# Kernel optimization log

Measured on AMD Instinct MI355X. Metric: run time of the kernel, lower is better.

## Reference

```python
import jax, jax.numpy as jnp
import numpy as np

# dims: B=batch, S=seq len, H=heads, D=in_features per head, R=realizations, K=conv kernel
B, S, H, D, R, K = 2, 1024, 8, 64, 32, 128


def setup_inputs() -> dict:
    key = jax.random.key(0)
    kq, kk, kwq, kwk, kz = jax.random.split(key, 5)
    queries = jax.random.normal(kq, (B, S, H, D), jnp.float32)
    keys = jax.random.normal(kk, (B, S, H, D), jnp.float32)
    # depthwise conv weights, torch init: uniform[0,1), shape (C_out, 1, K) with groups=C_out
    wq = jax.random.uniform(kwq, (H * D, 1, K), jnp.float32)
    wk = jax.random.uniform(kwk, (H * D, 1, K), jnp.float32)
    # stochastic process noise z: (B*R, H*D, 4K+S), scaled by 1/sqrt(R*D)
    z = jax.random.normal(kz, (B * R, H * D, 4 * K + S), jnp.float32) / np.float32(np.sqrt(R * D))
    return {"queries": queries, "keys": keys, "wq": wq, "wk": wk, "z": z}


def _dwconv(x, w):
    # depthwise 1D cross-correlation, VALID padding (matches nn.Conv1d, groups=C)
    return jax.lax.conv_general_dilated(
        x, w, window_strides=(1,), padding='VALID',
        dimension_numbers=('NCH', 'OIH', 'NCH'),
        feature_group_count=w.shape[0])


def reference(queries, keys, wq, wk, z):
    # note the faithful swap from the source: kbar uses conv_q, qbar uses conv_k
    kbar = _dwconv(z, wq)[:, :, K:K + S].reshape(B, R, H, D, S)
    qbar = _dwconv(z, wk)[:, :, K:K + S].reshape(B, R, H, D, S)
    # fused broadcast-multiply + feature-dim reduction:
    # (qbar * queries[:,None]).sum(axis=3) then permute -> (B,S,H,R)
    qhat = jnp.einsum('brhds,bshd->bshr', qbar, queries)
    khat = jnp.einsum('brhds,bshd->bshr', kbar, keys)
    return qhat, khat
```

## Files before the change

### kernel.cpp

```cpp
#include <hip/hip_runtime.h>

#define BB 2
#define SS 1024
#define HH 8
#define DD 64
#define RR 32
#define KK 128
#define ZLEN 1536
#define HD 512

#define MS 256
#define DC 16
#define NTC 24
#define WROWS 192
#define WSEG (WROWS*DC)
#define PARTS_FLOATS (256*8*2*64*16)

typedef _Float16 f16x8 __attribute__((ext_vector_type(8)));
typedef _Float16 f16x2 __attribute__((ext_vector_type(2)));
typedef float    f32x16 __attribute__((ext_vector_type(16)));

__global__ __launch_bounds__(1024) void convspe_mfma(
    const float* __restrict__ q, const float* __restrict__ kmat,
    const float* __restrict__ wq, const float* __restrict__ wk,
    const float* __restrict__ z, float* __restrict__ parts)
{
    __shared__ __align__(16) _Float16 zbuf[2][16 * 32 * 16];
    __shared__ __align__(16) _Float16 wqs[WSEG];
    __shared__ __align__(16) _Float16 wks[WSEG];

    const int tid  = threadIdx.x;
    const int wv   = tid >> 6;
    const int ssub = __builtin_amdgcn_readfirstlane(wv & 7);
    const int half = __builtin_amdgcn_readfirstlane(wv >> 3);
    const int lane = tid & 63;
    const int rl   = lane & 31;
    const int hi   = lane >> 5;

    const int bx = blockIdx.x;
    const int dc = bx & 3, stile = (bx >> 2) & 3, h = (bx >> 4) & 7, b = bx >> 7;
    const int s0b = stile * MS;
    const int d0  = dc * DC;

    const int sr  = tid >> 5;
    const int sdp = (tid >> 2) & 7;
    const int sth = tid & 3;
    const float* zr0 = z + ((size_t)(b * RR + sr) * HD + h * DD + d0 + 2 * sdp) * ZLEN
                         + KK + s0b + sth * 4;
    const float* zr1 = zr0 + ZLEN;

    float4 ra, rb;
    auto loadchunk = [&](int tc) {
        ra = *(const float4*)(zr0 + tc * 16);
        rb = *(const float4*)(zr1 + tc * 16);
    };
    auto writechunk = [&](int p) {
        f16x2* dst = (f16x2*)zbuf[p];
        const float av[4] = {ra.x, ra.y, ra.z, ra.w};
        const float bv[4] = {rb.x, rb.y, rb.z, rb.w};
        #pragma unroll
        for (int e = 0; e < 4; ++e) {
            const int ts = sth * 4 + e;
            dst[(ts * 32 + sr) * 8 + sdp] =
                __builtin_bit_cast(f16x2, __builtin_amdgcn_cvt_pkrtz(av[e], bv[e]));
        }
    };

    loadchunk(0);

    f16x8 qf, kf;
    {
        const int s = s0b + ssub * 32 + rl;
        const size_t base = (((size_t)b * SS + s) * HH + h) * DD + d0 + 8 * hi;
        #pragma unroll
        for (int j = 0; j < 8; ++j) {
            qf[j] = (_Float16)q[base + j];
            kf[j] = (_Float16)kmat[base + j];
        }
    }

    {
        const int t2 = tid & 511;
        const int di = t2 & 15, tq = t2 >> 4;
        const float* warr = (tid < 512) ? wq : wk;
        _Float16* wdst    = (tid < 512) ? wqs : wks;
        const float4 v4 = *(const float4*)&warr[(h * DD + dc * DC + di) * KK + tq * 4];
        const float av[4] = {v4.x, v4.y, v4.z, v4.w};
        #pragma unroll
        for (int e = 0; e < 4; ++e)
            wdst[(tq * 4 + e + 32) * 16 + di] = (_Float16)av[e];
        wdst[t2] = (_Float16)0.f;
        wdst[2560 + t2] = (_Float16)0.f;
    }

    f32x16 accq, acck;
    #pragma unroll
    for (int j = 0; j < 16; ++j) { accq[j] = 0.f; acck[j] = 0.f; }

    writechunk(0);
    loadchunk(1);
    __syncthreads();

    for (int tc = 0; tc < NTC; ++tc) {
        const int p = tc & 1;
        const int tqbase = tc * 16 - ssub * 32;
        const int lo  = (tqbase < 0) ? -tqbase : 0;
        const int hi_ = (160 - tqbase < 16) ? (160 - tqbase) : 16;
        const int ps  = lo + ((lo ^ half) & 1);
        if (ps < hi_) {
            const _Float16* zb = zbuf[p];
            auto zrd = [&](int ts) {
                return *(const f16x8*)&zb[(ts * 32 + rl) * 16 + 8 * hi];
            };
            auto wrd = [&](const _Float16* ws, int ts) {
                const int row = tqbase + ts - rl + 32;
                return *(const f16x8*)&ws[row * 16 + 8 * hi];
            };
            f16x8 a0 = zrd(ps), k0 = wrd(wks, ps), q0 = wrd(wqs, ps);
            f16x8 a1 = a0, k1 = k0, q1 = q0;
            if (ps + 2 < hi_) { a1 = zrd(ps + 2); k1 = wrd(wks, ps + 2); q1 = wrd(wqs, ps + 2); }
            for (int ts = ps; ts < hi_ - 4; ts += 2) {
                const f16x8 a2 = zrd(ts + 4), k2 = wrd(wks, ts + 4), q2 = wrd(wqs, ts + 4);
                accq = __builtin_amdgcn_mfma_f32_32x32x16_f16(a0, k0 * qf, accq, 0, 0, 0);
                acck = __builtin_amdgcn_mfma_f32_32x32x16_f16(a0, q0 * kf, acck, 0, 0, 0);
                a0 = a1; k0 = k1; q0 = q1;
                a1 = a2; k1 = k2; q1 = q2;
            }
            accq = __builtin_amdgcn_mfma_f32_32x32x16_f16(a0, k0 * qf, accq, 0, 0, 0);
            acck = __builtin_amdgcn_mfma_f32_32x32x16_f16(a0, q0 * kf, acck, 0, 0, 0);
            if (ps + 2 < hi_) {
                accq = __builtin_amdgcn_mfma_f32_32x32x16_f16(a1, k1 * qf, accq, 0, 0, 0);
                acck = __builtin_amdgcn_mfma_f32_32x32x16_f16(a1, q1 * kf, acck, 0, 0, 0);
            }
        }
        if (tc + 1 < NTC) writechunk((tc + 1) & 1);
        if (tc + 2 < NTC) loadchunk(tc + 2);
        __syncthreads();
    }

    {
        float* mrg = (float*)zbuf;
        const int col = ssub * 64 + lane;
        if (half == 1) {
            #pragma unroll
            for (int j = 0; j < 16; ++j) mrg[j * 512 + col] = accq[j];
        }
        __syncthreads();
        if (half == 0) {
            #pragma unroll
            for (int j = 0; j < 16; ++j) accq[j] += mrg[j * 512 + col];
        }
        __syncthreads();
        if (half == 1) {
            #pragma unroll
            for (int j = 0; j < 16; ++j) mrg[j * 512 + col] = acck[j];
        }
        __syncthreads();
        if (half == 0) {
            #pragma unroll
            for (int j = 0; j < 16; ++j) acck[j] += mrg[j * 512 + col];
        }
    }

    if (half == 0) {
        float* pq = parts + ((((size_t)bx * 8 + ssub) * 2 + 0) * 64 + lane) * 16;
        float* pk = parts + ((((size_t)bx * 8 + ssub) * 2 + 1) * 64 + lane) * 16;
        #pragma unroll
        for (int g = 0; g < 4; ++g) {
            *(float4*)&pq[g * 4] = make_float4(accq[4*g], accq[4*g+1], accq[4*g+2], accq[4*g+3]);
            *(float4*)&pk[g * 4] = make_float4(acck[4*g], acck[4*g+1], acck[4*g+2], acck[4*g+3]);
        }
    }
}

__global__ __launch_bounds__(256) void reduce_kernel(
    const float* __restrict__ parts, float* __restrict__ out)
{
    const int idx = blockIdx.x * 256 + threadIdx.x;
    const int rq = idx & 7, h = (idx >> 3) & 7, s = (idx >> 6) & 1023;
    const int b = (idx >> 16) & 1, o = idx >> 17;
    const int stile = s >> 8, sub = (s >> 5) & 7, rl = s & 31;

    const int off = ((rq & 1) * 32 + rl) * 16 + 4 * (rq >> 1);

    float4 acc = make_float4(0.f, 0.f, 0.f, 0.f);
    #pragma unroll
    for (int dc = 0; dc < 4; ++dc) {
        const int bx = ((b * 8 + h) * 4 + stile) * 4 + dc;
        const float4 v = *(const float4*)&parts[(((size_t)bx * 8 + sub) * 2 + o) * 1024 + off];
        acc.x += v.x; acc.y += v.y; acc.z += v.z; acc.w += v.w;
    }
    *(float4*)&out[(size_t)idx * 4] = acc;
}

extern "C" void kernel_launch(void* const* d_in, const int* in_sizes, int n_in,
                              void* d_out, int out_size, void* d_ws, size_t ws_size,
                              hipStream_t stream) {
    const float* q  = (const float*)d_in[0];
    const float* k  = (const float*)d_in[1];
    const float* wq = (const float*)d_in[2];
    const float* wk = (const float*)d_in[3];
    const float* z  = (const float*)d_in[4];
    float* out = (float*)d_out;

    float* parts = (float*)d_ws;

    hipLaunchKernelGGL(convspe_mfma, dim3(256), dim3(1024), 0, stream,
                       q, k, wq, wk, z, parts);
    hipLaunchKernelGGL(reduce_kernel, dim3(1024), dim3(256), 0, stream, parts, out);
}
```

Measured before the change: 300.2 us.

## Deepen z staging to four LDS buffers and sync once per two chunks

The z shared-memory staging grows from double to quadruple buffering, with two register sets in flight. The loop now processes two time chunks per iteration and needs only one barrier per pair, which halves the __syncthreads count and gives global loads more time to land before use. In exchange it doubles z LDS usage and adds registers, which could affect occupancy with 1024-thread blocks.

```diff
diff --git a/kernel.cpp b/kernel.cpp
--- a/kernel.cpp
+++ b/kernel.cpp
@@ -25,7 +25,7 @@
     const float* __restrict__ wq, const float* __restrict__ wk,
     const float* __restrict__ z, float* __restrict__ parts)
 {
-    __shared__ __align__(16) _Float16 zbuf[2][16 * 32 * 16];
+    __shared__ __align__(16) _Float16 zbuf[4][16 * 32 * 16];
     __shared__ __align__(16) _Float16 wqs[WSEG];
     __shared__ __align__(16) _Float16 wks[WSEG];
 
@@ -49,15 +49,15 @@
                          + KK + s0b + sth * 4;
     const float* zr1 = zr0 + ZLEN;
 
-    float4 ra, rb;
-    auto loadchunk = [&](int tc) {
-        ra = *(const float4*)(zr0 + tc * 16);
-        rb = *(const float4*)(zr1 + tc * 16);
+    float4 ra0, rb0, ra1, rb1;
+    auto loadch = [&](int tc, float4& a, float4& b) {
+        a = *(const float4*)(zr0 + tc * 16);
+        b = *(const float4*)(zr1 + tc * 16);
     };
-    auto writechunk = [&](int p) {
-        f16x2* dst = (f16x2*)zbuf[p];
-        const float av[4] = {ra.x, ra.y, ra.z, ra.w};
-        const float bv[4] = {rb.x, rb.y, rb.z, rb.w};
+    auto writech = [&](int tc, const float4& a, const float4& b) {
+        f16x2* dst = (f16x2*)zbuf[tc & 3];
+        const float av[4] = {a.x, a.y, a.z, a.w};
+        const float bv[4] = {b.x, b.y, b.z, b.w};
         #pragma unroll
         for (int e = 0; e < 4; ++e) {
             const int ts = sth * 4 + e;
@@ -66,7 +66,7 @@
         }
     };
 
-    loadchunk(0);
+    loadch(0, ra0, rb0);
 
     f16x8 qf, kf;
     {
@@ -97,44 +97,52 @@
     #pragma unroll
     for (int j = 0; j < 16; ++j) { accq[j] = 0.f; acck[j] = 0.f; }
 
-    writechunk(0);
-    loadchunk(1);
-    __syncthreads();
-
-    for (int tc = 0; tc < NTC; ++tc) {
-        const int p = tc & 1;
+    auto compute = [&](int tc) {
         const int tqbase = tc * 16 - ssub * 32;
         const int lo  = (tqbase < 0) ? -tqbase : 0;
         const int hi_ = (160 - tqbase < 16) ? (160 - tqbase) : 16;
         const int ps  = lo + ((lo ^ half) & 1);
-        if (ps < hi_) {
-            const _Float16* zb = zbuf[p];
-            auto zrd = [&](int ts) {
-                return *(const f16x8*)&zb[(ts * 32 + rl) * 16 + 8 * hi];
-            };
-            auto wrd = [&](const _Float16* ws, int ts) {
-                const int row = tqbase + ts - rl + 32;
-                return *(const f16x8*)&ws[row * 16 + 8 * hi];
-            };
-            f16x8 a0 = zrd(ps), k0 = wrd(wks, ps), q0 = wrd(wqs, ps);
-            f16x8 a1 = a0, k1 = k0, q1 = q0;
-            if (ps + 2 < hi_) { a1 = zrd(ps + 2); k1 = wrd(wks, ps + 2); q1 = wrd(wqs, ps + 2); }
-            for (int ts = ps; ts < hi_ - 4; ts += 2) {
-                const f16x8 a2 = zrd(ts + 4), k2 = wrd(wks, ts + 4), q2 = wrd(wqs, ts + 4);
-                accq = __builtin_amdgcn_mfma_f32_32x32x16_f16(a0, k0 * qf, accq, 0, 0, 0);
-                acck = __builtin_amdgcn_mfma_f32_32x32x16_f16(a0, q0 * kf, acck, 0, 0, 0);
-                a0 = a1; k0 = k1; q0 = q1;
-                a1 = a2; k1 = k2; q1 = q2;
-            }
+        if (ps >= hi_) return;
+        const _Float16* zb = zbuf[tc & 3];
+        auto zrd = [&](int ts) {
+            return *(const f16x8*)&zb[(ts * 32 + rl) * 16 + 8 * hi];
+        };
+        auto wrd = [&](const _Float16* ws, int ts) {
+            const int row = tqbase + ts - rl + 32;
+            return *(const f16x8*)&ws[row * 16 + 8 * hi];
+        };
+        f16x8 a0 = zrd(ps), k0 = wrd(wks, ps), q0 = wrd(wqs, ps);
+        f16x8 a1 = a0, k1 = k0, q1 = q0;
+        if (ps + 2 < hi_) { a1 = zrd(ps + 2); k1 = wrd(wks, ps + 2); q1 = wrd(wqs, ps + 2); }
+        for (int ts = ps; ts < hi_ - 4; ts += 2) {
+            const f16x8 a2 = zrd(ts + 4), k2 = wrd(wks, ts + 4), q2 = wrd(wqs, ts + 4);
             accq = __builtin_amdgcn_mfma_f32_32x32x16_f16(a0, k0 * qf, accq, 0, 0, 0);
             acck = __builtin_amdgcn_mfma_f32_32x32x16_f16(a0, q0 * kf, acck, 0, 0, 0);
-            if (ps + 2 < hi_) {
-                accq = __builtin_amdgcn_mfma_f32_32x32x16_f16(a1, k1 * qf, accq, 0, 0, 0);
-                acck = __builtin_amdgcn_mfma_f32_32x32x16_f16(a1, q1 * kf, acck, 0, 0, 0);
-            }
-        }
-        if (tc + 1 < NTC) writechunk((tc + 1) & 1);
-        if (tc + 2 < NTC) loadchunk(tc + 2);
+            a0 = a1; k0 = k1; q0 = q1;
+            a1 = a2; k1 = k2; q1 = q2;
+        }
+        accq = __builtin_amdgcn_mfma_f32_32x32x16_f16(a0, k0 * qf, accq, 0, 0, 0);
+        acck = __builtin_amdgcn_mfma_f32_32x32x16_f16(a0, q0 * kf, acck, 0, 0, 0);
+        if (ps + 2 < hi_) {
+            accq = __builtin_amdgcn_mfma_f32_32x32x16_f16(a1, k1 * qf, accq, 0, 0, 0);
+            acck = __builtin_amdgcn_mfma_f32_32x32x16_f16(a1, q1 * kf, acck, 0, 0, 0);
+        }
+    };
+
+    loadch(1, ra1, rb1);
+    writech(0, ra0, rb0);
+    loadch(2, ra0, rb0);
+    writech(1, ra1, rb1);
+    loadch(3, ra1, rb1);
+    __syncthreads();
+
+    for (int t2 = 0; t2 < NTC; t2 += 2) {
+        if (t2 + 2 < NTC) writech(t2 + 2, ra0, rb0);
+        if (t2 + 4 < NTC) loadch(t2 + 4, ra0, rb0);
+        compute(t2);
+        if (t2 + 3 < NTC) writech(t2 + 3, ra1, rb1);
+        if (t2 + 5 < NTC) loadch(t2 + 5, ra1, rb1);
+        compute(t2 + 1);
         __syncthreads();
     }
 
```

After: 303.6 us. About the same (+1.1%).
